# Kernel tuning notes

Hardware: AMD Instinct MI355X
Metric: run time of the kernel (lower is better)

Reference implementation:

```python
import jax, jax.numpy as jnp
import numpy as np


def _highway(x, Ws, bs):
    # Ws: [n_hw, 2H, H] (torch Linear layout), bs: [n_hw, 2H]
    H = x.shape[-1]
    for i in range(Ws.shape[0]):
        proj = jnp.einsum('bsh,oh->bso', x, Ws[i]) + bs[i]
        nonlin = jax.nn.relu(proj[..., :H])
        gate = jax.nn.sigmoid(proj[..., H:])
        x = gate * x + (1.0 - gate) * nonlin
    return x


def setup_inputs() -> dict:
    key = jax.random.key(0)
    ks = jax.random.split(key, 10)
    B, S, H, L, W, NHW = 32, 512, 512, 2, 4, 2
    scale = 1.0 / np.sqrt(H)
    return {
        'inputs': jax.random.normal(ks[0], (B, S, H), dtype=jnp.float32),
        'masks': jnp.ones((B, S), dtype=jnp.int32),
        'fwd_pads': jax.random.normal(ks[1], (L, W, H), dtype=jnp.float32) * scale,
        'bwd_pads': jax.random.normal(ks[2], (L, W, H), dtype=jnp.float32) * scale,
        'fwd_ws': jax.random.normal(ks[3], (L, W + 1), dtype=jnp.float32),
        'bwd_ws': jax.random.normal(ks[4], (L, W + 1), dtype=jnp.float32),
        'fwd_hw_W': jax.random.normal(ks[5], (L, NHW, 2 * H, H), dtype=jnp.float32) * scale,
        'fwd_hw_b': jax.random.normal(ks[6], (L, NHW, 2 * H), dtype=jnp.float32) * 0.1,
        'bwd_hw_W': jax.random.normal(ks[7], (L, NHW, 2 * H, H), dtype=jnp.float32) * scale,
        'bwd_hw_b': jax.random.normal(ks[8], (L, NHW, 2 * H), dtype=jnp.float32) * 0.1,
    }


def reference(inputs, masks, fwd_pads, bwd_pads, fwd_ws, bwd_ws,
              fwd_hw_W, fwd_hw_b, bwd_hw_W, bwd_hw_b):
    # inputs: [B,S,H]; masks unused (as in the torch module)
    B, S, H = inputs.shape
    L, W, _ = fwd_pads.shape
    fwd_in = inputs
    bwd_in = inputs
    outs = []
    for l in range(L):
        fp = jnp.broadcast_to(fwd_pads[l], (B, W, H))
        bp = jnp.broadcast_to(bwd_pads[l], (B, W, H))
        pf = jnp.concatenate([fp, fwd_in, bp], axis=1)  # [B, S+2W, H]
        pb = jnp.concatenate([fp, bwd_in, bp], axis=1)
        # forward window at t covers padded positions t..t+W (causal)
        f_win = jnp.stack([pf[:, k:k + S] for k in range(W + 1)], axis=0)  # [W+1,B,S,H]
        f_out = jnp.einsum('k,kbsh->bsh', fwd_ws[l], f_win)
        # backward window at t covers padded positions t+W..t+2W (anti-causal)
        b_win = jnp.stack([pb[:, W + k:W + k + S] for k in range(W + 1)], axis=0)
        b_out = jnp.einsum('k,kbsh->bsh', bwd_ws[l], b_win)
        f_out = _highway(f_out, fwd_hw_W[l], fwd_hw_b[l])
        b_out = _highway(b_out, bwd_hw_W[l], bwd_hw_b[l])
        fwd_in, bwd_in = f_out, b_out
        outs.append(jnp.concatenate([f_out, b_out], axis=-1))
    return jnp.stack(outs, axis=0)  # [L, B, S, 2H]
```

## Files before the change

### kernel.cpp

```cpp
#include <hip/hip_runtime.h>
#include <hip/hip_bf16.h>

typedef __attribute__((ext_vector_type(8))) short bf16x8;
typedef __attribute__((ext_vector_type(4))) float floatx4;

#define B_ 32
#define S_ 512
#define H_ 512
#define M_ (B_*S_)
#define K_ 512
#define N_ 1024

__device__ __forceinline__ void gload_lds16(const void* g, void* l) {
  __builtin_amdgcn_global_load_lds(
      (const __attribute__((address_space(1))) void*)g,
      (__attribute__((address_space(3))) void*)l, 16, 0, 0);
}

__global__ void cvt2_kernel(const float* __restrict__ s0, const float* __restrict__ s1,
                            __hip_bfloat16* __restrict__ d0, __hip_bfloat16* __restrict__ d1) {
  int t = blockIdx.x * 256 + threadIdx.x;
  const float* src;
  __hip_bfloat16* dst;
  int i;
  if (t < 524288) { src = s0; dst = d0; i = t; }
  else            { src = s1; dst = d1; i = t - 524288; }
  float4 v = *(const float4*)(src + (size_t)i * 4);
  union { ushort4 u; __hip_bfloat16 h[4]; } pk;
  pk.h[0] = __float2bfloat16(v.x);
  pk.h[1] = __float2bfloat16(v.y);
  pk.h[2] = __float2bfloat16(v.z);
  pk.h[3] = __float2bfloat16(v.w);
  *(ushort4*)((unsigned short*)dst + (size_t)i * 4) = pk.u;
}

__global__ void conv_kernel(const float* __restrict__ inf, const float* __restrict__ inb,
                            int instride,
                            const float* __restrict__ fpad, const float* __restrict__ bpad,
                            const float* __restrict__ fw, const float* __restrict__ bw,
                            __hip_bfloat16* __restrict__ xaf, __hip_bfloat16* __restrict__ xab) {
  int t = blockIdx.x * 256 + threadIdx.x;
  int dir = blockIdx.y;
  int row = t >> 7;
  int hv  = (t & 127) << 2;
  int s = row & (S_ - 1);
  float4 a = make_float4(0.f, 0.f, 0.f, 0.f);
  if (dir == 0) {
#pragma unroll
    for (int k = 0; k < 5; ++k) {
      float w = fw[k];
      const float* src = (s + k < 4) ? (fpad + (size_t)(s + k) * H_ + hv)
                                     : (inf + (size_t)(row + k - 4) * instride + hv);
      float4 v = *(const float4*)src;
      a.x += w * v.x; a.y += w * v.y; a.z += w * v.z; a.w += w * v.w;
    }
  } else {
#pragma unroll
    for (int k = 0; k < 5; ++k) {
      float w = bw[k];
      const float* src = (s + k < S_) ? (inb + (size_t)(row + k) * instride + hv)
                                      : (bpad + (size_t)(s + k - S_) * H_ + hv);
      float4 v = *(const float4*)src;
      a.x += w * v.x; a.y += w * v.y; a.z += w * v.z; a.w += w * v.w;
    }
  }
  __hip_bfloat16* xa = dir ? xab : xaf;
  union { ushort4 u; __hip_bfloat16 h[4]; } pk;
  pk.h[0] = __float2bfloat16(a.x);
  pk.h[1] = __float2bfloat16(a.y);
  pk.h[2] = __float2bfloat16(a.z);
  pk.h[3] = __float2bfloat16(a.w);
  *(ushort4*)((unsigned short*)xa + (size_t)row * H_ + hv) = pk.u;
}

__global__ __launch_bounds__(1024, 4)
void hw_gemm(const __hip_bfloat16* __restrict__ Af, const __hip_bfloat16* __restrict__ Ab,
             const __hip_bfloat16* __restrict__ Wf, const __hip_bfloat16* __restrict__ Wb,
             const float* __restrict__ biasf, const float* __restrict__ biasb,
             __hip_bfloat16* __restrict__ Anf, __hip_bfloat16* __restrict__ Anb,
             float* __restrict__ outp, int final_mode) {
  __shared__ __align__(16) char smem[65536];

  const int tid = threadIdx.x;
  const int lane = tid & 63, wave = tid >> 6;
  const int wm = wave >> 2, wn = wave & 3;
  const int quad = lane >> 4, l16 = lane & 15;
  const int dir = blockIdx.z;

  const int n = blockIdx.x;
  const int by = n & 63, bx = n >> 6;
  const int m0 = by * 256;
  const int h0 = bx * 128;

  const __hip_bfloat16* A = dir ? Ab : Af;
  const __hip_bfloat16* Wm = dir ? Wb : Wf;
  const float* bias = dir ? biasb : biasf;
  __hip_bfloat16* An = dir ? Anb : Anf;

  floatx4 acc[4][4];
#pragma unroll
  for (int i = 0; i < 4; ++i)
#pragma unroll
    for (int j = 0; j < 4; ++j) acc[i][j] = (floatx4){0.f, 0.f, 0.f, 0.f};

  const int srow = lane >> 2;
  const int skk  = (((lane & 3) ^ ((lane >> 3) & 3)) << 3);
  const int key  = (l16 >> 1) & 3;
  const int xkp  = bx * 4 + wn;

  const __hip_bfloat16* aptr = A + (size_t)(m0 + wave * 16 + srow) * K_ + skk;
  const int brow = wave * 16 + srow;
  const int wnp = brow >> 6, rr = brow & 63;
  const int wrow = (rr < 32) ? (h0 + wnp * 32 + rr)
                             : (512 + h0 + wnp * 32 + (rr - 32));
  const __hip_bfloat16* bptr = Wm + (size_t)wrow * K_ + skk;

  gload_lds16(aptr, smem + wave * 1024);
  gload_lds16(bptr, smem + 16384 + wave * 1024);
  __syncthreads();

  unsigned int xsp[4][2][2];
  int cur = 0;
  for (int kp = 0; kp < 16; ++kp) {
    const __hip_bfloat16* cA = (const __hip_bfloat16*)(smem + (cur << 15));
    const __hip_bfloat16* cB = (const __hip_bfloat16*)(smem + (cur << 15) + 16384);
    if (kp < 15) {
      char* nb = smem + ((cur ^ 1) << 15);
      const int kb = (kp + 1) * 32;
      gload_lds16(aptr + kb, nb + wave * 1024);
      gload_lds16(bptr + kb, nb + 16384 + wave * 1024);
    }
    if (kp == xkp) {
      const unsigned short* pA = (const unsigned short*)cA;
#pragma unroll
      for (int i = 0; i < 4; ++i)
#pragma unroll
        for (int jj = 0; jj < 2; ++jj)
#pragma unroll
          for (int rh = 0; rh < 2; ++rh) {
            const int ra0 = wm * 64 + i * 16 + quad * 4 + rh * 2;
            const int ra1 = ra0 + 1;
            const int c2 = jj * 16 + l16;
            unsigned int lo = pA[ra0 * 32 + ((((c2 >> 3) ^ ((ra0 >> 1) & 3)) << 3) | (c2 & 7))];
            unsigned int hi = pA[ra1 * 32 + ((((c2 >> 3) ^ ((ra1 >> 1) & 3)) << 3) | (c2 & 7))];
            xsp[i][jj][rh] = lo | (hi << 16);
          }
    }
    bf16x8 av[4], bv[4];
#pragma unroll
    for (int i = 0; i < 4; ++i) {
      const int ra = wm * 64 + i * 16 + l16;
      av[i] = *(const bf16x8*)&cA[ra * 32 + ((quad ^ key) << 3)];
    }
#pragma unroll
    for (int j = 0; j < 4; ++j) {
      const int rb = wn * 64 + j * 16 + l16;
      bv[j] = *(const bf16x8*)&cB[rb * 32 + ((quad ^ key) << 3)];
    }
#pragma unroll
    for (int i = 0; i < 4; ++i)
#pragma unroll
      for (int j = 0; j < 4; ++j)
        acc[i][j] = __builtin_amdgcn_mfma_f32_16x16x32_bf16(av[i], bv[j], acc[i][j], 0, 0, 0);

    __syncthreads();
    cur ^= 1;
  }

  float bnl[2], bgt[2];
#pragma unroll
  for (int j = 0; j < 2; ++j) {
    const int c = h0 + wn * 32 + j * 16 + l16;
    bnl[j] = bias[c];
    bgt[j] = bias[512 + c];
  }

  if (final_mode) {
    float* ft = (float*)smem;
#pragma unroll
    for (int p = 0; p < 2; ++p) {
      if ((wn >> 1) == p) {
#pragma unroll
        for (int i = 0; i < 4; ++i)
#pragma unroll
          for (int r = 0; r < 4; ++r) {
            const int rl = wm * 64 + i * 16 + quad * 4 + r;
#pragma unroll
            for (int j = 0; j < 2; ++j) {
              float pn = acc[i][j][r] + bnl[j];
              float pg = acc[i][j + 2][r] + bgt[j];
              float g = 1.f / (1.f + __expf(-pg));
              unsigned int u = xsp[i][j][r >> 1];
              unsigned int bits = (r & 1) ? (u >> 16) : (u & 0xffffu);
              float xo = __uint_as_float(bits << 16);
              ft[rl * 64 + (wn & 1) * 32 + j * 16 + l16] =
                  g * xo + (1.f - g) * fmaxf(pn, 0.f);
            }
          }
      }
      __syncthreads();
#pragma unroll
      for (int q = 0; q < 4; ++q) {
        const int rl = q * 64 + (tid >> 4);
        const int cc = (tid & 15) * 4;
        float4 v = *(const float4*)&ft[rl * 64 + cc];
        *(float4*)&outp[(size_t)(m0 + rl) * N_ + dir * H_ + h0 + p * 64 + cc] = v;
      }
      __syncthreads();
    }
  } else {
    __hip_bfloat16* bt = (__hip_bfloat16*)smem;
#pragma unroll
    for (int i = 0; i < 4; ++i)
#pragma unroll
      for (int r = 0; r < 4; ++r) {
        const int rl = wm * 64 + i * 16 + quad * 4 + r;
#pragma unroll
        for (int j = 0; j < 2; ++j) {
          float pn = acc[i][j][r] + bnl[j];
          float pg = acc[i][j + 2][r] + bgt[j];
          float g = 1.f / (1.f + __expf(-pg));
          unsigned int u = xsp[i][j][r >> 1];
          unsigned int bits = (r & 1) ? (u >> 16) : (u & 0xffffu);
          float xo = __uint_as_float(bits << 16);
          bt[rl * 128 + wn * 32 + j * 16 + l16] =
              __float2bfloat16(g * xo + (1.f - g) * fmaxf(pn, 0.f));
        }
      }
    __syncthreads();
    const unsigned short* src = (const unsigned short*)smem;
#pragma unroll
    for (int q = 0; q < 4; ++q) {
      const int rl = q * 64 + (tid >> 4);
      const int cc = (tid & 15) * 8;
      int4 v = *(const int4*)(src + rl * 128 + cc);
      *(int4*)((unsigned short*)An + (size_t)(m0 + rl) * H_ + h0 + cc) = v;
    }
  }
}

extern "C" void kernel_launch(void* const* d_in, const int* in_sizes, int n_in,
                              void* d_out, int out_size, void* d_ws, size_t ws_size,
                              hipStream_t stream) {
  const float* inputs   = (const float*)d_in[0];
  const float* fwd_pads = (const float*)d_in[2];
  const float* bwd_pads = (const float*)d_in[3];
  const float* fwd_ws_p = (const float*)d_in[4];
  const float* bwd_ws_p = (const float*)d_in[5];
  const float* fwd_hw_W = (const float*)d_in[6];
  const float* fwd_hw_b = (const float*)d_in[7];
  const float* bwd_hw_W = (const float*)d_in[8];
  const float* bwd_hw_b = (const float*)d_in[9];
  float* out = (float*)d_out;

  char* ws = (char*)d_ws;
  size_t off = 0;
  __hip_bfloat16* Wbf = (__hip_bfloat16*)(ws + off); off += (size_t)4194304 * 2;
  __hip_bfloat16* xa0f = (__hip_bfloat16*)(ws + off); off += (size_t)M_ * H_ * 2;
  __hip_bfloat16* xa0b = (__hip_bfloat16*)(ws + off); off += (size_t)M_ * H_ * 2;
  __hip_bfloat16* xa1f = (__hip_bfloat16*)(ws + off); off += (size_t)M_ * H_ * 2;
  __hip_bfloat16* xa1b = (__hip_bfloat16*)(ws + off); off += (size_t)M_ * H_ * 2;

  cvt2_kernel<<<4096, 256, 0, stream>>>(fwd_hw_W, bwd_hw_W, Wbf, Wbf + (size_t)2097152);

  for (int l = 0; l < 2; ++l) {
    const float *inf, *inb;
    int instride;
    if (l == 0) { inf = inputs; inb = inputs; instride = H_; }
    else        { inf = out;    inb = out + H_; instride = N_; }
    conv_kernel<<<dim3(8192, 2), 256, 0, stream>>>(
        inf, inb, instride,
        fwd_pads + (size_t)l * 4 * H_, bwd_pads + (size_t)l * 4 * H_,
        fwd_ws_p + l * 5, bwd_ws_p + l * 5,
        xa0f, xa0b);

    hw_gemm<<<dim3(256, 1, 2), 1024, 0, stream>>>(
        xa0f, xa0b,
        Wbf + (size_t)(l * 2) * 524288, Wbf + (size_t)2097152 + (size_t)(l * 2) * 524288,
        fwd_hw_b + (l * 2) * 1024, bwd_hw_b + (l * 2) * 1024,
        xa1f, xa1b, nullptr, 0);

    hw_gemm<<<dim3(256, 1, 2), 1024, 0, stream>>>(
        xa1f, xa1b,
        Wbf + (size_t)(l * 2 + 1) * 524288, Wbf + (size_t)2097152 + (size_t)(l * 2 + 1) * 524288,
        fwd_hw_b + (l * 2 + 1) * 1024, bwd_hw_b + (l * 2 + 1) * 1024,
        nullptr, nullptr, out + (size_t)l * M_ * N_, 1);
  }
}
```

Baseline: 460.7 us.

## Retile highway GEMM to 128-row blocks with 64-wide K steps and grouped ordering

Measured after the change: 440.0 us. -4.5%, faster.

```diff
diff --git a/kernel.cpp b/kernel.cpp
--- a/kernel.cpp
+++ b/kernel.cpp
@@ -73,13 +73,13 @@
   *(ushort4*)((unsigned short*)xa + (size_t)row * H_ + hv) = pk.u;
 }
 
-__global__ __launch_bounds__(1024, 4)
+__global__ __launch_bounds__(512, 4)
 void hw_gemm(const __hip_bfloat16* __restrict__ Af, const __hip_bfloat16* __restrict__ Ab,
              const __hip_bfloat16* __restrict__ Wf, const __hip_bfloat16* __restrict__ Wb,
              const float* __restrict__ biasf, const float* __restrict__ biasb,
              __hip_bfloat16* __restrict__ Anf, __hip_bfloat16* __restrict__ Anb,
              float* __restrict__ outp, int final_mode) {
-  __shared__ __align__(16) char smem[65536];
+  __shared__ __align__(16) char smem[49152];
 
   const int tid = threadIdx.x;
   const int lane = tid & 63, wave = tid >> 6;
@@ -88,8 +88,9 @@
   const int dir = blockIdx.z;
 
   const int n = blockIdx.x;
-  const int by = n & 63, bx = n >> 6;
-  const int m0 = by * 256;
+  const int mpanel = (n & 7) | ((n >> 5) << 3);
+  const int bx = (n >> 3) & 3;
+  const int m0 = mpanel * 128;
   const int h0 = bx * 128;
 
   const __hip_bfloat16* A = dir ? Ab : Af;
@@ -97,41 +98,50 @@
   const float* bias = dir ? biasb : biasf;
   __hip_bfloat16* An = dir ? Anb : Anf;
 
+  __hip_bfloat16* lA = (__hip_bfloat16*)smem;
+  __hip_bfloat16* lB = (__hip_bfloat16*)(smem + 16384);
+
   floatx4 acc[4][4];
 #pragma unroll
   for (int i = 0; i < 4; ++i)
 #pragma unroll
     for (int j = 0; j < 4; ++j) acc[i][j] = (floatx4){0.f, 0.f, 0.f, 0.f};
 
-  const int srow = lane >> 2;
-  const int skk  = (((lane & 3) ^ ((lane >> 3) & 3)) << 3);
-  const int key  = (l16 >> 1) & 3;
-  const int xkp  = bx * 4 + wn;
-
-  const __hip_bfloat16* aptr = A + (size_t)(m0 + wave * 16 + srow) * K_ + skk;
-  const int brow = wave * 16 + srow;
-  const int wnp = brow >> 6, rr = brow & 63;
-  const int wrow = (rr < 32) ? (h0 + wnp * 32 + rr)
-                             : (512 + h0 + wnp * 32 + (rr - 32));
-  const __hip_bfloat16* bptr = Wm + (size_t)wrow * K_ + skk;
-
-  gload_lds16(aptr, smem + wave * 1024);
-  gload_lds16(bptr, smem + 16384 + wave * 1024);
-  __syncthreads();
+  const int srow = lane >> 3;
+  const int skk  = (((lane & 7) ^ srow) << 3);
+  const int xkp  = bx * 2 + (wn >> 1);
+
+  const __hip_bfloat16* aptr[2];
+#pragma unroll
+  for (int c = 0; c < 2; ++c) {
+    const int chunk = wave * 2 + c;
+    aptr[c] = A + (size_t)(m0 + chunk * 8 + srow) * K_ + skk;
+  }
+  const __hip_bfloat16* bptr[4];
+#pragma unroll
+  for (int c = 0; c < 4; ++c) {
+    const int chunk = wave * 4 + c;
+    const int brow = chunk * 8 + srow;
+    const int wnp = brow >> 6, rr = brow & 63;
+    const int wrow = (rr < 32) ? (h0 + wnp * 32 + rr)
+                               : (512 + h0 + wnp * 32 + (rr - 32));
+    bptr[c] = Wm + (size_t)wrow * K_ + skk;
+  }
 
   unsigned int xsp[4][2][2];
-  int cur = 0;
-  for (int kp = 0; kp < 16; ++kp) {
-    const __hip_bfloat16* cA = (const __hip_bfloat16*)(smem + (cur << 15));
-    const __hip_bfloat16* cB = (const __hip_bfloat16*)(smem + (cur << 15) + 16384);
-    if (kp < 15) {
-      char* nb = smem + ((cur ^ 1) << 15);
-      const int kb = (kp + 1) * 32;
-      gload_lds16(aptr + kb, nb + wave * 1024);
-      gload_lds16(bptr + kb, nb + 16384 + wave * 1024);
-    }
+
+  for (int kp = 0; kp < 8; ++kp) {
+    const int kb = kp * 64;
+#pragma unroll
+    for (int c = 0; c < 2; ++c)
+      gload_lds16(aptr[c] + kb, smem + (wave * 2 + c) * 1024);
+#pragma unroll
+    for (int c = 0; c < 4; ++c)
+      gload_lds16(bptr[c] + kb, smem + 16384 + (wave * 4 + c) * 1024);
+    __syncthreads();
+
     if (kp == xkp) {
-      const unsigned short* pA = (const unsigned short*)cA;
+      const unsigned short* pA = (const unsigned short*)lA;
 #pragma unroll
       for (int i = 0; i < 4; ++i)
 #pragma unroll
@@ -140,31 +150,33 @@
           for (int rh = 0; rh < 2; ++rh) {
             const int ra0 = wm * 64 + i * 16 + quad * 4 + rh * 2;
             const int ra1 = ra0 + 1;
-            const int c2 = jj * 16 + l16;
-            unsigned int lo = pA[ra0 * 32 + ((((c2 >> 3) ^ ((ra0 >> 1) & 3)) << 3) | (c2 & 7))];
-            unsigned int hi = pA[ra1 * 32 + ((((c2 >> 3) ^ ((ra1 >> 1) & 3)) << 3) | (c2 & 7))];
+            const int c2 = (wn & 1) * 32 + jj * 16 + l16;
+            unsigned int lo = pA[ra0 * 64 + ((((c2 >> 3) ^ (ra0 & 7)) << 3) | (c2 & 7))];
+            unsigned int hi = pA[ra1 * 64 + ((((c2 >> 3) ^ (ra1 & 7)) << 3) | (c2 & 7))];
             xsp[i][jj][rh] = lo | (hi << 16);
           }
     }
-    bf16x8 av[4], bv[4];
-#pragma unroll
-    for (int i = 0; i < 4; ++i) {
-      const int ra = wm * 64 + i * 16 + l16;
-      av[i] = *(const bf16x8*)&cA[ra * 32 + ((quad ^ key) << 3)];
-    }
-#pragma unroll
-    for (int j = 0; j < 4; ++j) {
-      const int rb = wn * 64 + j * 16 + l16;
-      bv[j] = *(const bf16x8*)&cB[rb * 32 + ((quad ^ key) << 3)];
-    }
-#pragma unroll
-    for (int i = 0; i < 4; ++i)
-#pragma unroll
-      for (int j = 0; j < 4; ++j)
-        acc[i][j] = __builtin_amdgcn_mfma_f32_16x16x32_bf16(av[i], bv[j], acc[i][j], 0, 0, 0);
-
+
+#pragma unroll
+    for (int ks = 0; ks < 2; ++ks) {
+      bf16x8 av[4], bv[4];
+#pragma unroll
+      for (int i = 0; i < 4; ++i) {
+        const int ra = wm * 64 + i * 16 + l16;
+        av[i] = *(const bf16x8*)&lA[ra * 64 + (((ks * 4 + quad) ^ (ra & 7)) << 3)];
+      }
+#pragma unroll
+      for (int j = 0; j < 4; ++j) {
+        const int rb = wn * 64 + j * 16 + l16;
+        bv[j] = *(const bf16x8*)&lB[rb * 64 + (((ks * 4 + quad) ^ (rb & 7)) << 3)];
+      }
+#pragma unroll
+      for (int i = 0; i < 4; ++i)
+#pragma unroll
+        for (int j = 0; j < 4; ++j)
+          acc[i][j] = __builtin_amdgcn_mfma_f32_16x16x32_bf16(av[i], bv[j], acc[i][j], 0, 0, 0);
+    }
     __syncthreads();
-    cur ^= 1;
   }
 
   float bnl[2], bgt[2];
@@ -201,7 +213,7 @@
       __syncthreads();
 #pragma unroll
       for (int q = 0; q < 4; ++q) {
-        const int rl = q * 64 + (tid >> 4);
+        const int rl = q * 32 + (tid >> 4);
         const int cc = (tid & 15) * 4;
         float4 v = *(const float4*)&ft[rl * 64 + cc];
         *(float4*)&outp[(size_t)(m0 + rl) * N_ + dir * H_ + h0 + p * 64 + cc] = v;
@@ -230,8 +242,8 @@
     __syncthreads();
     const unsigned short* src = (const unsigned short*)smem;
 #pragma unroll
-    for (int q = 0; q < 4; ++q) {
-      const int rl = q * 64 + (tid >> 4);
+    for (int p = 0; p < 4; ++p) {
+      const int rl = p * 32 + (tid >> 4);
       const int cc = (tid & 15) * 8;
       int4 v = *(const int4*)(src + rl * 128 + cc);
       *(int4*)((unsigned short*)An + (size_t)(m0 + rl) * H_ + h0 + cc) = v;
@@ -274,13 +286,13 @@
         fwd_ws_p + l * 5, bwd_ws_p + l * 5,
         xa0f, xa0b);
 
-    hw_gemm<<<dim3(256, 1, 2), 1024, 0, stream>>>(
+    hw_gemm<<<dim3(512, 1, 2), 512, 0, stream>>>(
         xa0f, xa0b,
         Wbf + (size_t)(l * 2) * 524288, Wbf + (size_t)2097152 + (size_t)(l * 2) * 524288,
         fwd_hw_b + (l * 2) * 1024, bwd_hw_b + (l * 2) * 1024,
         xa1f, xa1b, nullptr, 0);
 
-    hw_gemm<<<dim3(256, 1, 2), 1024, 0, stream>>>(
+    hw_gemm<<<dim3(512, 1, 2), 512, 0, stream>>>(
         xa1f, xa1b,
         Wbf + (size_t)(l * 2 + 1) * 524288, Wbf + (size_t)2097152 + (size_t)(l * 2 + 1) * 524288,
         fwd_hw_b + (l * 2 + 1) * 1024, bwd_hw_b + (l * 2 + 1) * 1024,
```
